# Performance work log

Hardware: AMD Instinct MI355X
Metric: run time of the kernel (lower is better)

## Reference

```python
import jax, jax.numpy as jnp
import numpy as np

N_NODES = 50000
N_EDGES = 800000
NUM_GRAPHS = 512


def gcn_conv(x, edge_index, W, b, num_nodes):
    # PyG GCNConv: h = D^{-1/2} (A + I) D^{-1/2} (x @ W) + b
    h = x @ W
    src, dst = edge_index[0], edge_index[1]
    loop = jnp.arange(num_nodes)
    src = jnp.concatenate([src, loop])
    dst = jnp.concatenate([dst, loop])
    deg = jax.ops.segment_sum(jnp.ones_like(dst, dtype=h.dtype), dst,
                              num_segments=num_nodes)
    dinv = jnp.where(deg > 0, jax.lax.rsqrt(deg), 0.0)
    norm = dinv[src] * dinv[dst]                      # [E+N]
    msg = h[src] * norm[:, None]                      # gather + scale
    out = jax.ops.segment_sum(msg, dst, num_segments=num_nodes)  # scatter-add
    return out + b


def global_mean_pool(x, batch, num_graphs):
    sums = jax.ops.segment_sum(x, batch, num_segments=num_graphs)
    cnts = jax.ops.segment_sum(jnp.ones((x.shape[0],), x.dtype), batch,
                               num_segments=num_graphs)
    return sums / jnp.maximum(cnts, 1.0)[:, None]


def setup_inputs() -> dict:
    key = jax.random.key(0)
    ks = jax.random.split(key, 8)
    x = jax.random.normal(ks[0], (N_NODES, 128), dtype=jnp.float32)
    edge_index = jax.random.randint(ks[1], (2, N_EDGES), 0, N_NODES, dtype=jnp.int64)
    batch = jnp.sort(jax.random.randint(ks[2], (N_NODES,), 0, NUM_GRAPHS, dtype=jnp.int64))
    W1 = jax.random.normal(ks[3], (128, 128), dtype=jnp.float32) * (1.0 / np.sqrt(128))
    b1 = jnp.zeros((128,), jnp.float32)
    W2 = jax.random.normal(ks[4], (128, 64), dtype=jnp.float32) * (1.0 / np.sqrt(128))
    b2 = jnp.zeros((64,), jnp.float32)
    Wl = jax.random.normal(ks[5], (64, 64), dtype=jnp.float32) * (1.0 / np.sqrt(64))
    bl = jnp.zeros((64,), jnp.float32)
    return {"x": x, "edge_index": edge_index, "batch": batch,
            "W1": W1, "b1": b1, "W2": W2, "b2": b2, "Wl": Wl, "bl": bl}


def reference(x, edge_index, batch, W1, b1, W2, b2, Wl, bl):
    num_nodes = x.shape[0]
    h = gcn_conv(x, edge_index, W1, b1, num_nodes)
    h = jax.nn.relu(h)
    h = gcn_conv(h, edge_index, W2, b2, num_nodes)
    g = global_mean_pool(h, batch, NUM_GRAPHS)
    # dropout p=0.5 is identity in eval mode
    return g @ Wl + bl
```

## Files before the change

kernel.cpp:

```cpp
#include <hip/hip_runtime.h>
#include <hip/hip_fp16.h>
#include <math.h>


#define FEAT1 128
#define FEAT2 64
#define BCAP 8192

using half8 = __attribute__((ext_vector_type(8))) _Float16;
using half4 = __attribute__((ext_vector_type(4))) _Float16;
using f32x4 = __attribute__((ext_vector_type(4))) float;


__global__ __launch_bounds__(256) void bin_scatter(const int* __restrict__ esrc,
                                                   const int* __restrict__ edst,
                                                   int ne, int nb,
                                                   int* __restrict__ bucket_cursor,
                                                   int* __restrict__ ebin) {
    __shared__ int lcnt[256];
    __shared__ int lcur[256];
    const int tid = threadIdx.x;
    const int e0 = blockIdx.x * 8192;
    lcnt[tid] = 0;
    __syncthreads();
    #pragma unroll 4
    for (int k = 0; k < 32; k++) {
        int e = e0 + k * 256 + tid;
        if (e < ne) atomicAdd(&lcnt[edst[e] >> 8], 1);
    }
    __syncthreads();
    if (tid < nb && lcnt[tid] > 0)
        lcur[tid] = atomicAdd(&bucket_cursor[tid], lcnt[tid]);
    __syncthreads();
    #pragma unroll 4
    for (int k = 0; k < 32; k++) {
        int e = e0 + k * 256 + tid;
        if (e < ne) {
            int d = edst[e];
            int b = d >> 8;
            int p = atomicAdd(&lcur[b], 1);
            if (p < BCAP)
                ebin[b * BCAP + p] = esrc[e] | ((d & 255) << 18);
        }
    }
}

__global__ __launch_bounds__(256) void bucket_csr(const int* __restrict__ ebin,
                                                  const int* __restrict__ bucket_cursor,
                                                  int n_nodes,
                                                  int* __restrict__ csr,
                                                  int2* __restrict__ nodeinfo,
                                                  float* __restrict__ dinv) {
    __shared__ int lcnt[256];
    __shared__ int lscan[256];
    __shared__ int lcur[256];
    const int b = blockIdx.x;
    const int tid = threadIdx.x;
    const int ebeg = b * BCAP;
    int cnt_b = bucket_cursor[b];
    if (cnt_b > BCAP) cnt_b = BCAP;
    const int eend = ebeg + cnt_b;
    lcnt[tid] = 0;
    __syncthreads();
    for (int e = ebeg + tid; e < eend; e += 256)
        atomicAdd(&lcnt[(ebin[e] >> 18) & 255], 1);
    __syncthreads();
    int v = lcnt[tid];
    lscan[tid] = v;
    __syncthreads();
    for (int off = 1; off < 256; off <<= 1) {
        int u = (tid >= off) ? lscan[tid - off] : 0;
        __syncthreads();
        lscan[tid] += u;
        __syncthreads();
    }
    const int start = ebeg + (lscan[tid] - v);
    const int node = (b << 8) + tid;
    if (node < n_nodes) {
        nodeinfo[node] = make_int2(start, v);
        dinv[node] = (float)(1.0 / sqrt((double)(v + 1)));
    }
    lcur[tid] = start;
    __syncthreads();
    for (int e = ebeg + tid; e < eend; e += 256) {
        int pk = ebin[e];
        int p = atomicAdd(&lcur[(pk >> 18) & 255], 1);
        csr[p] = pk & 0x3FFFF;
    }
}

template <int FOUT, bool A_F16>
__global__ __launch_bounds__(256) void gemm_mfma(const void* __restrict__ Aptr,
                                                 const float* __restrict__ W,
                                                 const float* __restrict__ dinv,
                                                 _Float16* __restrict__ out, int n) {
    __shared__ _Float16 As[128 * 136];
    __shared__ _Float16 Ws[64 * 136];
    const int tid = threadIdx.x;
    const int wv = tid >> 6;
    const int lane = tid & 63;
    constexpr int NCT = FOUT / 64;
    const int row0 = (blockIdx.x / NCT) * 128;
    const int col0 = (blockIdx.x % NCT) * 64;

    {
        const int r = tid >> 1;
        const int c0 = (tid & 1) * 64;
        const int grow = row0 + r;
        if constexpr (A_F16) {
            const _Float16* A = (const _Float16*)Aptr + (size_t)grow * 128 + c0;
            #pragma unroll
            for (int j = 0; j < 8; j++) {
                half8 v = {};
                if (grow < n) v = *(const half8*)(A + j * 8);
                *(half8*)(&As[r * 136 + c0 + j * 8]) = v;
            }
        } else {
            const float* A = (const float*)Aptr + (size_t)grow * 128 + c0;
            #pragma unroll
            for (int j = 0; j < 16; j++) {
                float4 v = {0.f, 0.f, 0.f, 0.f};
                if (grow < n) v = *(const float4*)(A + j * 4);
                half4 hv = {(_Float16)v.x, (_Float16)v.y, (_Float16)v.z, (_Float16)v.w};
                *(half4*)(&As[r * 136 + c0 + j * 4]) = hv;
            }
        }
    }
    {
        const int k = tid >> 1;
        const int cb = (tid & 1) * 32;
        #pragma unroll
        for (int j = 0; j < 8; j++) {
            int c = cb + j * 4;
            float4 v = *(const float4*)(W + (size_t)k * FOUT + col0 + c);
            Ws[(c + 0) * 136 + k] = (_Float16)v.x;
            Ws[(c + 1) * 136 + k] = (_Float16)v.y;
            Ws[(c + 2) * 136 + k] = (_Float16)v.z;
            Ws[(c + 3) * 136 + k] = (_Float16)v.w;
        }
    }
    __syncthreads();

    f32x4 acc[2][4] = {};
    const int mrow = wv * 32 + (lane & 15);
    const int kb = (lane >> 4) * 8;
    #pragma unroll
    for (int ks = 0; ks < 4; ks++) {
        const int kk = ks * 32 + kb;
        half8 a0 = *(const half8*)(&As[mrow * 136 + kk]);
        half8 a1 = *(const half8*)(&As[(mrow + 16) * 136 + kk]);
        #pragma unroll
        for (int nj = 0; nj < 4; nj++) {
            half8 b = *(const half8*)(&Ws[(nj * 16 + (lane & 15)) * 136 + kk]);
            acc[0][nj] = __builtin_amdgcn_mfma_f32_16x16x32_f16(a0, b, acc[0][nj], 0, 0, 0);
            acc[1][nj] = __builtin_amdgcn_mfma_f32_16x16x32_f16(a1, b, acc[1][nj], 0, 0, 0);
        }
    }

    #pragma unroll
    for (int mi = 0; mi < 2; mi++) {
        const int gr0 = row0 + wv * 32 + mi * 16 + (lane >> 4) * 4;
        #pragma unroll
        for (int r = 0; r < 4; r++) {
            const int grow = gr0 + r;
            if (grow < n) {
                const float s = dinv[grow];
                #pragma unroll
                for (int nj = 0; nj < 4; nj++) {
                    out[(size_t)grow * FOUT + col0 + nj * 16 + (lane & 15)] =
                        (_Float16)(acc[mi][nj][r] * s);
                }
            }
        }
    }
}

template <int F, bool RELU, bool OUT16>
__global__ __launch_bounds__(256) void aggregate_h(const __half* __restrict__ t,
                                                   const float* __restrict__ dinv,
                                                   const int2* __restrict__ nodeinfo,
                                                   const int* __restrict__ csr_src,
                                                   const float* __restrict__ bias,
                                                   void* __restrict__ outp, int n) {
    const int wv = threadIdx.x >> 6;
    const int lane = threadIdx.x & 63;
    const int i = blockIdx.x * 4 + wv;
    if (i >= n) return;
    const float di = dinv[i];
    const int2 ni = nodeinfo[i];
    const int e0 = ni.x, e1 = ni.x + ni.y;

    if constexpr (F == 128) {
        float2 a0, a1 = {0.f, 0.f}, a2 = {0.f, 0.f}, a3 = {0.f, 0.f};
        a0 = __half22float2(((const __half2*)(t + (size_t)i * F))[lane]);
        int e = e0;
        for (; e + 4 <= e1; e += 4) {
            int s0 = csr_src[e + 0], s1 = csr_src[e + 1], s2 = csr_src[e + 2], s3 = csr_src[e + 3];
            float2 v0 = __half22float2(((const __half2*)(t + (size_t)s0 * F))[lane]);
            float2 v1 = __half22float2(((const __half2*)(t + (size_t)s1 * F))[lane]);
            float2 v2 = __half22float2(((const __half2*)(t + (size_t)s2 * F))[lane]);
            float2 v3 = __half22float2(((const __half2*)(t + (size_t)s3 * F))[lane]);
            a0.x += v0.x; a0.y += v0.y;
            a1.x += v1.x; a1.y += v1.y;
            a2.x += v2.x; a2.y += v2.y;
            a3.x += v3.x; a3.y += v3.y;
        }
        for (; e < e1; e++) {
            int s = csr_src[e];
            float2 v = __half22float2(((const __half2*)(t + (size_t)s * F))[lane]);
            a0.x += v.x; a0.y += v.y;
        }
        float2 b = ((const float2*)bias)[lane];
        float rx = (a0.x + a1.x + a2.x + a3.x) * di + b.x;
        float ry = (a0.y + a1.y + a2.y + a3.y) * di + b.y;
        if (RELU) { rx = fmaxf(rx, 0.f); ry = fmaxf(ry, 0.f); }
        if constexpr (OUT16) {
            ((__half2*)((__half*)outp + (size_t)i * F))[lane] = __floats2half2_rn(rx, ry);
        } else {
            ((float2*)((float*)outp + (size_t)i * F))[lane] = make_float2(rx, ry);
        }
    } else {
        float a0, a1 = 0.f, a2 = 0.f, a3 = 0.f;
        a0 = __half2float(t[(size_t)i * F + lane]);
        int e = e0;
        for (; e + 4 <= e1; e += 4) {
            int s0 = csr_src[e + 0], s1 = csr_src[e + 1], s2 = csr_src[e + 2], s3 = csr_src[e + 3];
            float v0 = __half2float(t[(size_t)s0 * F + lane]);
            float v1 = __half2float(t[(size_t)s1 * F + lane]);
            float v2 = __half2float(t[(size_t)s2 * F + lane]);
            float v3 = __half2float(t[(size_t)s3 * F + lane]);
            a0 += v0; a1 += v1; a2 += v2; a3 += v3;
        }
        for (; e < e1; e++) {
            a0 += __half2float(t[(size_t)csr_src[e] * F + lane]);
        }
        float r = (a0 + a1 + a2 + a3) * di + bias[lane];
        if (RELU) r = fmaxf(r, 0.f);
        if constexpr (OUT16) {
            ((__half*)outp)[(size_t)i * F + lane] = __float2half(r);
        } else {
            ((float*)outp)[(size_t)i * F + lane] = r;
        }
    }
}

__global__ __launch_bounds__(256) void pool_classify(const float* __restrict__ h2,
                                                     const int* __restrict__ batch, int n,
                                                     const float* __restrict__ Wl,
                                                     const float* __restrict__ bl,
                                                     float* __restrict__ out) {
    __shared__ float partial[4][64];
    __shared__ float pooled_s[64];
    const int g = blockIdx.x;
    const int wv = threadIdx.x >> 6;
    const int lane = threadIdx.x & 63;

    int lo = 0, hi = n;
    while (lo < hi) { int mid = (lo + hi) >> 1; if (batch[mid] < g) lo = mid + 1; else hi = mid; }
    const int start = lo;
    hi = n;
    while (lo < hi) { int mid = (lo + hi) >> 1; if (batch[mid] < g + 1) lo = mid + 1; else hi = mid; }
    const int end = lo;

    float sum = 0.0f;
    int r = start + wv;
    for (; r + 8 <= end; r += 8) {
        float v0 = h2[(size_t)r * 64 + lane];
        float v1 = h2[(size_t)(r + 4) * 64 + lane];
        sum += v0 + v1;
    }
    for (; r < end; r += 4) sum += h2[(size_t)r * 64 + lane];
    partial[wv][lane] = sum;
    __syncthreads();

    if (wv == 0) {
        float s = partial[0][lane] + partial[1][lane] + partial[2][lane] + partial[3][lane];
        float cnt = (float)(end - start);
        pooled_s[lane] = s / fmaxf(cnt, 1.0f);
    }
    __syncthreads();

    if (wv == 0) {
        float acc = bl[lane];
        #pragma unroll 8
        for (int k = 0; k < 64; k++) acc += pooled_s[k] * Wl[k * 64 + lane];
        out[(size_t)g * 64 + lane] = acc;
    }
}


extern "C" void kernel_launch(void* const* d_in, const int* in_sizes, int n_in,
                              void* d_out, int out_size, void* d_ws, size_t ws_size,
                              hipStream_t stream) {
    const float* x    = (const float*)d_in[0];
    const int*   eidx = (const int*)d_in[1];
    const int*   batch= (const int*)d_in[2];
    const float* W1   = (const float*)d_in[3];
    const float* b1   = (const float*)d_in[4];
    const float* W2   = (const float*)d_in[5];
    const float* b2   = (const float*)d_in[6];
    const float* Wl   = (const float*)d_in[7];
    const float* bl   = (const float*)d_in[8];
    float* out = (float*)d_out;

    const int n_nodes  = in_sizes[0] / FEAT1;
    const int n_edges  = in_sizes[1] / 2;
    const int n_graphs = out_size / FEAT2;
    const int* esrc = eidx;
    const int* edst = eidx + n_edges;
    const int nb = (n_nodes + 255) >> 8;

    char* ws = (char*)d_ws;
    size_t off = 0;
    auto alloc = [&](size_t bytes) -> void* {
        void* p = ws + off;
        off += (bytes + 255) & ~(size_t)255;
        return p;
    };
    _Float16* t1     = (_Float16*)alloc((size_t)n_nodes * FEAT1 * 2);
    __half*   h1h    = (__half*)alloc((size_t)n_nodes * FEAT1 * 2);
    float*    h2     = (float*)alloc((size_t)n_nodes * FEAT2 * 4);
    float*    dinv   = (float*)alloc((size_t)n_nodes * 4);
    int2*   nodeinfo = (int2*)alloc((size_t)n_nodes * 8);
    int*    bcur     = (int*)alloc((size_t)nb * 4);
    int*    ebin     = (int*)alloc((size_t)nb * BCAP * 4);
    int*    csr      = (int*)alloc((size_t)nb * BCAP * 4);

    const int nrb = (n_nodes + 127) / 128;

    hipMemsetAsync(bcur, 0, (size_t)nb * 4, stream);
    bin_scatter<<<(n_edges + 8191) / 8192, 256, 0, stream>>>(esrc, edst, n_edges, nb, bcur, ebin);
    bucket_csr<<<nb, 256, 0, stream>>>(ebin, bcur, n_nodes, csr, nodeinfo, dinv);

    gemm_mfma<FEAT1, false><<<nrb * (FEAT1 / 64), 256, 0, stream>>>(x, W1, dinv, t1, n_nodes);
    aggregate_h<FEAT1, true, true><<<(n_nodes + 3) / 4, 256, 0, stream>>>(
        (const __half*)t1, dinv, nodeinfo, csr, b1, h1h, n_nodes);

    gemm_mfma<FEAT2, true><<<nrb * (FEAT2 / 64), 256, 0, stream>>>(h1h, W2, dinv, t1, n_nodes);
    aggregate_h<FEAT2, false, false><<<(n_nodes + 3) / 4, 256, 0, stream>>>(
        (const __half*)t1, dinv, nodeinfo, csr, b2, h2, n_nodes);

    pool_classify<<<n_graphs, 256, 0, stream>>>(h2, batch, n_nodes, Wl, bl, out);
}
```

Measured before the change: 169.5 us.

## Partition transformed features into 32-column planes for cache-local gather aggregation

The GEMM now writes its fp16 output as separate 32-column planes (one per feature slice) and loops over column tiles inside one block instead of splitting tiles across blocks. Aggregation becomes a 2D grid over nodes and planes, where each wavefront handles four edges at once with 16 lanes per 64-byte row and combines the partial sums with shuffles. The intent is to shrink each pass's gather working set so it fits in cache and to make gathers use whole row segments. The cost is repeated reads of CSR and node info for every plane, some idle lanes in the tail loop, and a GEMM grid with fewer blocks.

Result: slower. 213.3 us (+25.9%).

```diff
diff --git a/kernel.cpp b/kernel.cpp
--- a/kernel.cpp
+++ b/kernel.cpp
@@ -93,15 +93,15 @@
 __global__ __launch_bounds__(256) void gemm_mfma(const void* __restrict__ Aptr,
                                                  const float* __restrict__ W,
                                                  const float* __restrict__ dinv,
-                                                 _Float16* __restrict__ out, int n) {
+                                                 _Float16* __restrict__ out,
+                                                 size_t pstride, int n) {
     __shared__ _Float16 As[128 * 136];
     __shared__ _Float16 Ws[64 * 136];
     const int tid = threadIdx.x;
     const int wv = tid >> 6;
     const int lane = tid & 63;
     constexpr int NCT = FOUT / 64;
-    const int row0 = (blockIdx.x / NCT) * 128;
-    const int col0 = (blockIdx.x % NCT) * 64;
+    const int row0 = blockIdx.x * 128;
 
     {
         const int r = tid >> 1;
@@ -126,120 +126,127 @@
             }
         }
     }
-    {
-        const int k = tid >> 1;
-        const int cb = (tid & 1) * 32;
+
+    for (int ct = 0; ct < NCT; ct++) {
+        const int col0 = ct * 64;
+        __syncthreads();
+        {
+            const int k = tid >> 1;
+            const int cb = (tid & 1) * 32;
+            #pragma unroll
+            for (int j = 0; j < 8; j++) {
+                int c = cb + j * 4;
+                float4 v = *(const float4*)(W + (size_t)k * FOUT + col0 + c);
+                Ws[(c + 0) * 136 + k] = (_Float16)v.x;
+                Ws[(c + 1) * 136 + k] = (_Float16)v.y;
+                Ws[(c + 2) * 136 + k] = (_Float16)v.z;
+                Ws[(c + 3) * 136 + k] = (_Float16)v.w;
+            }
+        }
+        __syncthreads();
+
+        f32x4 acc[2][4] = {};
+        const int mrow = wv * 32 + (lane & 15);
+        const int kb = (lane >> 4) * 8;
         #pragma unroll
-        for (int j = 0; j < 8; j++) {
-            int c = cb + j * 4;
-            float4 v = *(const float4*)(W + (size_t)k * FOUT + col0 + c);
-            Ws[(c + 0) * 136 + k] = (_Float16)v.x;
-            Ws[(c + 1) * 136 + k] = (_Float16)v.y;
-            Ws[(c + 2) * 136 + k] = (_Float16)v.z;
-            Ws[(c + 3) * 136 + k] = (_Float16)v.w;
-        }
-    }
-    __syncthreads();
-
-    f32x4 acc[2][4] = {};
-    const int mrow = wv * 32 + (lane & 15);
-    const int kb = (lane >> 4) * 8;
-    #pragma unroll
-    for (int ks = 0; ks < 4; ks++) {
-        const int kk = ks * 32 + kb;
-        half8 a0 = *(const half8*)(&As[mrow * 136 + kk]);
-        half8 a1 = *(const half8*)(&As[(mrow + 16) * 136 + kk]);
+        for (int ks = 0; ks < 4; ks++) {
+            const int kk = ks * 32 + kb;
+            half8 a0 = *(const half8*)(&As[mrow * 136 + kk]);
+            half8 a1 = *(const half8*)(&As[(mrow + 16) * 136 + kk]);
+            #pragma unroll
+            for (int nj = 0; nj < 4; nj++) {
+                half8 b = *(const half8*)(&Ws[(nj * 16 + (lane & 15)) * 136 + kk]);
+                acc[0][nj] = __builtin_amdgcn_mfma_f32_16x16x32_f16(a0, b, acc[0][nj], 0, 0, 0);
+                acc[1][nj] = __builtin_amdgcn_mfma_f32_16x16x32_f16(a1, b, acc[1][nj], 0, 0, 0);
+            }
+        }
+
         #pragma unroll
-        for (int nj = 0; nj < 4; nj++) {
-            half8 b = *(const half8*)(&Ws[(nj * 16 + (lane & 15)) * 136 + kk]);
-            acc[0][nj] = __builtin_amdgcn_mfma_f32_16x16x32_f16(a0, b, acc[0][nj], 0, 0, 0);
-            acc[1][nj] = __builtin_amdgcn_mfma_f32_16x16x32_f16(a1, b, acc[1][nj], 0, 0, 0);
-        }
-    }
-
-    #pragma unroll
-    for (int mi = 0; mi < 2; mi++) {
-        const int gr0 = row0 + wv * 32 + mi * 16 + (lane >> 4) * 4;
-        #pragma unroll
-        for (int r = 0; r < 4; r++) {
-            const int grow = gr0 + r;
-            if (grow < n) {
-                const float s = dinv[grow];
-                #pragma unroll
-                for (int nj = 0; nj < 4; nj++) {
-                    out[(size_t)grow * FOUT + col0 + nj * 16 + (lane & 15)] =
-                        (_Float16)(acc[mi][nj][r] * s);
+        for (int mi = 0; mi < 2; mi++) {
+            const int gr0 = row0 + wv * 32 + mi * 16 + (lane >> 4) * 4;
+            #pragma unroll
+            for (int r = 0; r < 4; r++) {
+                const int grow = gr0 + r;
+                if (grow < n) {
+                    const float s = dinv[grow];
+                    #pragma unroll
+                    for (int nj = 0; nj < 4; nj++) {
+                        const int col = col0 + nj * 16 + (lane & 15);
+                        out[(size_t)(col >> 5) * pstride + (size_t)grow * 32 + (col & 31)] =
+                            (_Float16)(acc[mi][nj][r] * s);
+                    }
                 }
             }
         }
     }
 }
 
-template <int F, bool RELU, bool OUT16>
-__global__ __launch_bounds__(256) void aggregate_h(const __half* __restrict__ t,
+template <bool RELU, bool OUT16>
+__global__ __launch_bounds__(256) void aggregate_p(const _Float16* __restrict__ tp,
+                                                   size_t pstride,
                                                    const float* __restrict__ dinv,
                                                    const int2* __restrict__ nodeinfo,
                                                    const int* __restrict__ csr_src,
                                                    const float* __restrict__ bias,
-                                                   void* __restrict__ outp, int n) {
+                                                   void* __restrict__ outp,
+                                                   int F, int n) {
     const int wv = threadIdx.x >> 6;
     const int lane = threadIdx.x & 63;
     const int i = blockIdx.x * 4 + wv;
     if (i >= n) return;
+    const int p = blockIdx.y;
+    const _Float16* t = tp + (size_t)p * pstride;
+    const int sub = lane >> 4;
+    const int sl = lane & 15;
+
     const float di = dinv[i];
     const int2 ni = nodeinfo[i];
     const int e0 = ni.x, e1 = ni.x + ni.y;
 
-    if constexpr (F == 128) {
-        float2 a0, a1 = {0.f, 0.f}, a2 = {0.f, 0.f}, a3 = {0.f, 0.f};
-        a0 = __half22float2(((const __half2*)(t + (size_t)i * F))[lane]);
-        int e = e0;
-        for (; e + 4 <= e1; e += 4) {
-            int s0 = csr_src[e + 0], s1 = csr_src[e + 1], s2 = csr_src[e + 2], s3 = csr_src[e + 3];
-            float2 v0 = __half22float2(((const __half2*)(t + (size_t)s0 * F))[lane]);
-            float2 v1 = __half22float2(((const __half2*)(t + (size_t)s1 * F))[lane]);
-            float2 v2 = __half22float2(((const __half2*)(t + (size_t)s2 * F))[lane]);
-            float2 v3 = __half22float2(((const __half2*)(t + (size_t)s3 * F))[lane]);
-            a0.x += v0.x; a0.y += v0.y;
-            a1.x += v1.x; a1.y += v1.y;
-            a2.x += v2.x; a2.y += v2.y;
-            a3.x += v3.x; a3.y += v3.y;
-        }
-        for (; e < e1; e++) {
-            int s = csr_src[e];
-            float2 v = __half22float2(((const __half2*)(t + (size_t)s * F))[lane]);
-            a0.x += v.x; a0.y += v.y;
-        }
-        float2 b = ((const float2*)bias)[lane];
-        float rx = (a0.x + a1.x + a2.x + a3.x) * di + b.x;
-        float ry = (a0.y + a1.y + a2.y + a3.y) * di + b.y;
+    float2 a0, a1 = {0.f, 0.f}, a2 = {0.f, 0.f}, a3 = {0.f, 0.f};
+    {
+        float2 v = {0.f, 0.f};
+        if (sub == 0) v = __half22float2(*(const __half2*)(t + (size_t)i * 32 + sl * 2));
+        a0 = v;
+    }
+
+    int e = e0;
+    for (; e + 16 <= e1; e += 16) {
+        int sA = csr_src[e + sub];
+        int sB = csr_src[e + 4 + sub];
+        int sC = csr_src[e + 8 + sub];
+        int sD = csr_src[e + 12 + sub];
+        float2 vA = __half22float2(*(const __half2*)(t + (size_t)sA * 32 + sl * 2));
+        float2 vB = __half22float2(*(const __half2*)(t + (size_t)sB * 32 + sl * 2));
+        float2 vC = __half22float2(*(const __half2*)(t + (size_t)sC * 32 + sl * 2));
+        float2 vD = __half22float2(*(const __half2*)(t + (size_t)sD * 32 + sl * 2));
+        a0.x += vA.x; a0.y += vA.y;
+        a1.x += vB.x; a1.y += vB.y;
+        a2.x += vC.x; a2.y += vC.y;
+        a3.x += vD.x; a3.y += vD.y;
+    }
+    for (; e < e1; e += 4) {
+        bool pr = (e + sub) < e1;
+        int s = pr ? csr_src[e + sub] : 0;
+        float2 v = {0.f, 0.f};
+        if (pr) v = __half22float2(*(const __half2*)(t + (size_t)s * 32 + sl * 2));
+        a0.x += v.x; a0.y += v.y;
+    }
+
+    float ax = a0.x + a1.x + a2.x + a3.x;
+    float ay = a0.y + a1.y + a2.y + a3.y;
+    ax += __shfl_xor(ax, 16); ay += __shfl_xor(ay, 16);
+    ax += __shfl_xor(ax, 32); ay += __shfl_xor(ay, 32);
+
+    if (sub == 0) {
+        float2 b = ((const float2*)(bias + p * 32))[sl];
+        float rx = ax * di + b.x;
+        float ry = ay * di + b.y;
         if (RELU) { rx = fmaxf(rx, 0.f); ry = fmaxf(ry, 0.f); }
         if constexpr (OUT16) {
-            ((__half2*)((__half*)outp + (size_t)i * F))[lane] = __floats2half2_rn(rx, ry);
+            ((__half2*)((__half*)outp + (size_t)i * F + p * 32))[sl] = __floats2half2_rn(rx, ry);
         } else {
-            ((float2*)((float*)outp + (size_t)i * F))[lane] = make_float2(rx, ry);
-        }
-    } else {
-        float a0, a1 = 0.f, a2 = 0.f, a3 = 0.f;
-        a0 = __half2float(t[(size_t)i * F + lane]);
-        int e = e0;
-        for (; e + 4 <= e1; e += 4) {
-            int s0 = csr_src[e + 0], s1 = csr_src[e + 1], s2 = csr_src[e + 2], s3 = csr_src[e + 3];
-            float v0 = __half2float(t[(size_t)s0 * F + lane]);
-            float v1 = __half2float(t[(size_t)s1 * F + lane]);
-            float v2 = __half2float(t[(size_t)s2 * F + lane]);
-            float v3 = __half2float(t[(size_t)s3 * F + lane]);
-            a0 += v0; a1 += v1; a2 += v2; a3 += v3;
-        }
-        for (; e < e1; e++) {
-            a0 += __half2float(t[(size_t)csr_src[e] * F + lane]);
-        }
-        float r = (a0 + a1 + a2 + a3) * di + bias[lane];
-        if (RELU) r = fmaxf(r, 0.f);
-        if constexpr (OUT16) {
-            ((__half*)outp)[(size_t)i * F + lane] = __float2half(r);
-        } else {
-            ((float*)outp)[(size_t)i * F + lane] = r;
+            ((float2*)((float*)outp + (size_t)i * F + p * 32))[sl] = make_float2(rx, ry);
         }
     }
 }
@@ -309,6 +316,7 @@
     const int* esrc = eidx;
     const int* edst = eidx + n_edges;
     const int nb = (n_nodes + 255) >> 8;
+    const size_t pstride = (size_t)n_nodes * 32;
 
     char* ws = (char*)d_ws;
     size_t off = 0;
@@ -327,18 +335,19 @@
     int*    csr      = (int*)alloc((size_t)nb * BCAP * 4);
 
     const int nrb = (n_nodes + 127) / 128;
+    const int nab = (n_nodes + 3) / 4;
 
     hipMemsetAsync(bcur, 0, (size_t)nb * 4, stream);
     bin_scatter<<<(n_edges + 8191) / 8192, 256, 0, stream>>>(esrc, edst, n_edges, nb, bcur, ebin);
     bucket_csr<<<nb, 256, 0, stream>>>(ebin, bcur, n_nodes, csr, nodeinfo, dinv);
 
-    gemm_mfma<FEAT1, false><<<nrb * (FEAT1 / 64), 256, 0, stream>>>(x, W1, dinv, t1, n_nodes);
-    aggregate_h<FEAT1, true, true><<<(n_nodes + 3) / 4, 256, 0, stream>>>(
-        (const __half*)t1, dinv, nodeinfo, csr, b1, h1h, n_nodes);
-
-    gemm_mfma<FEAT2, true><<<nrb * (FEAT2 / 64), 256, 0, stream>>>(h1h, W2, dinv, t1, n_nodes);
-    aggregate_h<FEAT2, false, false><<<(n_nodes + 3) / 4, 256, 0, stream>>>(
-        (const __half*)t1, dinv, nodeinfo, csr, b2, h2, n_nodes);
+    gemm_mfma<FEAT1, false><<<nrb, 256, 0, stream>>>(x, W1, dinv, t1, pstride, n_nodes);
+    aggregate_p<true, true><<<dim3(nab, FEAT1 / 32), 256, 0, stream>>>(
+        t1, pstride, dinv, nodeinfo, csr, b1, h1h, FEAT1, n_nodes);
+
+    gemm_mfma<FEAT2, true><<<nrb, 256, 0, stream>>>(h1h, W2, dinv, t1, pstride, n_nodes);
+    aggregate_p<false, false><<<dim3(nab, FEAT2 / 32), 256, 0, stream>>>(
+        t1, pstride, dinv, nodeinfo, csr, b2, h2, FEAT2, n_nodes);
 
     pool_classify<<<n_graphs, 256, 0, stream>>>(h2, batch, n_nodes, Wl, bl, out);
 }
```

## Loop GEMM column tiles inside one block and unroll aggregation gathers by eight

Applied to the files above, without the earlier changes.

The MFMA GEMM now has each block load its 128-row A tile once and loop over all 64-column output tiles, restaging W each time. Before, the A tile was read separately for every column tile, so for the first layer x was read twice from global memory. The aggregation kernels also unroll the neighbor gather loop to eight edges per iteration, which keeps more independent loads in flight. The costs are half as many GEMM blocks for layer one, serialized column tiles with extra barriers, and higher register pressure in the aggregation loop.

Measured after the change: 152.9 us. -9.8%, faster.

```diff
diff --git a/kernel.cpp b/kernel.cpp
--- a/kernel.cpp
+++ b/kernel.cpp
@@ -100,8 +100,7 @@
     const int wv = tid >> 6;
     const int lane = tid & 63;
     constexpr int NCT = FOUT / 64;
-    const int row0 = (blockIdx.x / NCT) * 128;
-    const int col0 = (blockIdx.x % NCT) * 64;
+    const int row0 = blockIdx.x * 128;
 
     {
         const int r = tid >> 1;
@@ -126,49 +125,54 @@
             }
         }
     }
-    {
-        const int k = tid >> 1;
-        const int cb = (tid & 1) * 32;
+
+    for (int ct = 0; ct < NCT; ct++) {
+        const int col0 = ct * 64;
+        __syncthreads();
+        {
+            const int k = tid >> 1;
+            const int cb = (tid & 1) * 32;
+            #pragma unroll
+            for (int j = 0; j < 8; j++) {
+                int c = cb + j * 4;
+                float4 v = *(const float4*)(W + (size_t)k * FOUT + col0 + c);
+                Ws[(c + 0) * 136 + k] = (_Float16)v.x;
+                Ws[(c + 1) * 136 + k] = (_Float16)v.y;
+                Ws[(c + 2) * 136 + k] = (_Float16)v.z;
+                Ws[(c + 3) * 136 + k] = (_Float16)v.w;
+            }
+        }
+        __syncthreads();
+
+        f32x4 acc[2][4] = {};
+        const int mrow = wv * 32 + (lane & 15);
+        const int kb = (lane >> 4) * 8;
         #pragma unroll
-        for (int j = 0; j < 8; j++) {
-            int c = cb + j * 4;
-            float4 v = *(const float4*)(W + (size_t)k * FOUT + col0 + c);
-            Ws[(c + 0) * 136 + k] = (_Float16)v.x;
-            Ws[(c + 1) * 136 + k] = (_Float16)v.y;
-            Ws[(c + 2) * 136 + k] = (_Float16)v.z;
-            Ws[(c + 3) * 136 + k] = (_Float16)v.w;
-        }
-    }
-    __syncthreads();
-
-    f32x4 acc[2][4] = {};
-    const int mrow = wv * 32 + (lane & 15);
-    const int kb = (lane >> 4) * 8;
-    #pragma unroll
-    for (int ks = 0; ks < 4; ks++) {
-        const int kk = ks * 32 + kb;
-        half8 a0 = *(const half8*)(&As[mrow * 136 + kk]);
-        half8 a1 = *(const half8*)(&As[(mrow + 16) * 136 + kk]);
+        for (int ks = 0; ks < 4; ks++) {
+            const int kk = ks * 32 + kb;
+            half8 a0 = *(const half8*)(&As[mrow * 136 + kk]);
+            half8 a1 = *(const half8*)(&As[(mrow + 16) * 136 + kk]);
+            #pragma unroll
+            for (int nj = 0; nj < 4; nj++) {
+                half8 b = *(const half8*)(&Ws[(nj * 16 + (lane & 15)) * 136 + kk]);
+                acc[0][nj] = __builtin_amdgcn_mfma_f32_16x16x32_f16(a0, b, acc[0][nj], 0, 0, 0);
+                acc[1][nj] = __builtin_amdgcn_mfma_f32_16x16x32_f16(a1, b, acc[1][nj], 0, 0, 0);
+            }
+        }
+
         #pragma unroll
-        for (int nj = 0; nj < 4; nj++) {
-            half8 b = *(const half8*)(&Ws[(nj * 16 + (lane & 15)) * 136 + kk]);
-            acc[0][nj] = __builtin_amdgcn_mfma_f32_16x16x32_f16(a0, b, acc[0][nj], 0, 0, 0);
-            acc[1][nj] = __builtin_amdgcn_mfma_f32_16x16x32_f16(a1, b, acc[1][nj], 0, 0, 0);
-        }
-    }
-
-    #pragma unroll
-    for (int mi = 0; mi < 2; mi++) {
-        const int gr0 = row0 + wv * 32 + mi * 16 + (lane >> 4) * 4;
-        #pragma unroll
-        for (int r = 0; r < 4; r++) {
-            const int grow = gr0 + r;
-            if (grow < n) {
-                const float s = dinv[grow];
-                #pragma unroll
-                for (int nj = 0; nj < 4; nj++) {
-                    out[(size_t)grow * FOUT + col0 + nj * 16 + (lane & 15)] =
-                        (_Float16)(acc[mi][nj][r] * s);
+        for (int mi = 0; mi < 2; mi++) {
+            const int gr0 = row0 + wv * 32 + mi * 16 + (lane >> 4) * 4;
+            #pragma unroll
+            for (int r = 0; r < 4; r++) {
+                const int grow = gr0 + r;
+                if (grow < n) {
+                    const float s = dinv[grow];
+                    #pragma unroll
+                    for (int nj = 0; nj < 4; nj++) {
+                        out[(size_t)grow * FOUT + col0 + nj * 16 + (lane & 15)] =
+                            (_Float16)(acc[mi][nj][r] * s);
+                    }
                 }
             }
         }
@@ -194,6 +198,22 @@
         float2 a0, a1 = {0.f, 0.f}, a2 = {0.f, 0.f}, a3 = {0.f, 0.f};
         a0 = __half22float2(((const __half2*)(t + (size_t)i * F))[lane]);
         int e = e0;
+        for (; e + 8 <= e1; e += 8) {
+            int s0 = csr_src[e + 0], s1 = csr_src[e + 1], s2 = csr_src[e + 2], s3 = csr_src[e + 3];
+            int s4 = csr_src[e + 4], s5 = csr_src[e + 5], s6 = csr_src[e + 6], s7 = csr_src[e + 7];
+            float2 v0 = __half22float2(((const __half2*)(t + (size_t)s0 * F))[lane]);
+            float2 v1 = __half22float2(((const __half2*)(t + (size_t)s1 * F))[lane]);
+            float2 v2 = __half22float2(((const __half2*)(t + (size_t)s2 * F))[lane]);
+            float2 v3 = __half22float2(((const __half2*)(t + (size_t)s3 * F))[lane]);
+            float2 v4 = __half22float2(((const __half2*)(t + (size_t)s4 * F))[lane]);
+            float2 v5 = __half22float2(((const __half2*)(t + (size_t)s5 * F))[lane]);
+            float2 v6 = __half22float2(((const __half2*)(t + (size_t)s6 * F))[lane]);
+            float2 v7 = __half22float2(((const __half2*)(t + (size_t)s7 * F))[lane]);
+            a0.x += v0.x + v4.x; a0.y += v0.y + v4.y;
+            a1.x += v1.x + v5.x; a1.y += v1.y + v5.y;
+            a2.x += v2.x + v6.x; a2.y += v2.y + v6.y;
+            a3.x += v3.x + v7.x; a3.y += v3.y + v7.y;
+        }
         for (; e + 4 <= e1; e += 4) {
             int s0 = csr_src[e + 0], s1 = csr_src[e + 1], s2 = csr_src[e + 2], s3 = csr_src[e + 3];
             float2 v0 = __half22float2(((const __half2*)(t + (size_t)s0 * F))[lane]);
@@ -223,13 +243,25 @@
         float a0, a1 = 0.f, a2 = 0.f, a3 = 0.f;
         a0 = __half2float(t[(size_t)i * F + lane]);
         int e = e0;
-        for (; e + 4 <= e1; e += 4) {
+        for (; e + 8 <= e1; e += 8) {
             int s0 = csr_src[e + 0], s1 = csr_src[e + 1], s2 = csr_src[e + 2], s3 = csr_src[e + 3];
+            int s4 = csr_src[e + 4], s5 = csr_src[e + 5], s6 = csr_src[e + 6], s7 = csr_src[e + 7];
             float v0 = __half2float(t[(size_t)s0 * F + lane]);
             float v1 = __half2float(t[(size_t)s1 * F + lane]);
             float v2 = __half2float(t[(size_t)s2 * F + lane]);
             float v3 = __half2float(t[(size_t)s3 * F + lane]);
-            a0 += v0; a1 += v1; a2 += v2; a3 += v3;
+            float v4 = __half2float(t[(size_t)s4 * F + lane]);
+            float v5 = __half2float(t[(size_t)s5 * F + lane]);
+            float v6 = __half2float(t[(size_t)s6 * F + lane]);
+            float v7 = __half2float(t[(size_t)s7 * F + lane]);
+            a0 += v0 + v4; a1 += v1 + v5; a2 += v2 + v6; a3 += v3 + v7;
+        }
+        for (; e + 4 <= e1; e += 4) {
+            int s0 = csr_src[e + 0], s1 = csr_src[e + 1], s2 = csr_src[e + 2], s3 = csr_src[e + 3];
+            a0 += __half2float(t[(size_t)s0 * F + lane]);
+            a1 += __half2float(t[(size_t)s1 * F + lane]);
+            a2 += __half2float(t[(size_t)s2 * F + lane]);
+            a3 += __half2float(t[(size_t)s3 * F + lane]);
         }
         for (; e < e1; e++) {
             a0 += __half2float(t[(size_t)csr_src[e] * F + lane]);
@@ -332,11 +364,11 @@
     bin_scatter<<<(n_edges + 8191) / 8192, 256, 0, stream>>>(esrc, edst, n_edges, nb, bcur, ebin);
     bucket_csr<<<nb, 256, 0, stream>>>(ebin, bcur, n_nodes, csr, nodeinfo, dinv);
 
-    gemm_mfma<FEAT1, false><<<nrb * (FEAT1 / 64), 256, 0, stream>>>(x, W1, dinv, t1, n_nodes);
+    gemm_mfma<FEAT1, false><<<nrb, 256, 0, stream>>>(x, W1, dinv, t1, n_nodes);
     aggregate_h<FEAT1, true, true><<<(n_nodes + 3) / 4, 256, 0, stream>>>(
         (const __half*)t1, dinv, nodeinfo, csr, b1, h1h, n_nodes);
 
-    gemm_mfma<FEAT2, true><<<nrb * (FEAT2 / 64), 256, 0, stream>>>(h1h, W2, dinv, t1, n_nodes);
+    gemm_mfma<FEAT2, true><<<nrb, 256, 0, stream>>>(h1h, W2, dinv, t1, n_nodes);
     aggregate_h<FEAT2, false, false><<<(n_nodes + 3) / 4, 256, 0, stream>>>(
         (const __half*)t1, dinv, nodeinfo, csr, b2, h2, n_nodes);
 
```
